# Kernel tuning notes

Hardware: AMD Instinct MI355X
Metric: run time of the kernel (lower is better)

The kernel has to match this reference:

```python
import jax, jax.numpy as jnp
import numpy as np


def _cdist(a, b):
    # Euclidean distance between rows of a [M,D] and b [K,D] -> [M,K]
    a2 = jnp.sum(a * a, axis=-1)[:, None]
    b2 = jnp.sum(b * b, axis=-1)[None, :]
    d2 = a2 + b2 - 2.0 * (a @ b.T)
    return jnp.sqrt(jnp.maximum(d2, 1e-12))


def setup_inputs() -> dict:
    key = jax.random.key(0)
    k1, k2, k3 = jax.random.split(key, 3)
    L, N1, N2, P, D = 2, 8, 8, 1024, 768  # 2 output layers, 32x32 patches, ViT-B dim
    feats = jax.random.normal(k1, (L, N1, P, D), dtype=jnp.float32)
    nfeats = jax.random.normal(k2, (L, N2, P, D), dtype=jnp.float32)
    background_mask = jax.random.uniform(k3, (N1, P), dtype=jnp.float32)
    return {
        "feats": feats,
        "nfeats": nfeats,
        "background_mask": background_mask,
        "img_h": 512,
        "img_w": 512,
        "patch_size": 16,
    }


def reference(feats, nfeats, background_mask, img_h, img_w, patch_size):
    L, N1, P, D = feats.shape
    N2 = nfeats.shape[1]
    PH = img_h // patch_size
    PW = img_w // patch_size

    # L2-normalize patch features (as in Model.forward)
    f = feats / jnp.linalg.norm(feats, axis=-1, keepdims=True)
    nf = nfeats / jnp.linalg.norm(nfeats, axis=-1, keepdims=True)

    scores_list, pixel_list = [], []
    for l in range(L):  # small fixed number of output layers
        a = f[l].reshape(N1 * P, D)
        b = nf[l].reshape(N2 * P, D)
        # [N1,P,N2,P] -> [N1,N2,P,P], halved as in the original
        d = _cdist(a, b).reshape(N1, P, N2, P).transpose(0, 2, 1, 3) / 2.0
        sp = jnp.min(d, axis=-1)                       # [N1,N2,P] nearest normal patch
        sp = sp * background_mask[:, None, :]          # mask background patches
        sc = jnp.mean(jnp.max(sp, axis=-1), axis=-1)   # [N1] image score
        spatch = jnp.mean(sp, axis=1).reshape(N1, PH, PW)
        # bilinear, align_corners=False (half-pixel centers)
        spix = jax.image.resize(spatch, (N1, img_h, img_w), method="bilinear")
        scores_list.append(sc)
        pixel_list.append(spix)

    scores = jnp.mean(jnp.stack(scores_list, axis=0), axis=0)        # [N1]
    scores_pixel = jnp.mean(jnp.stack(pixel_list, axis=0), axis=0)   # [N1,H,W]
    return scores, scores_pixel
```

## Files before the change

kernel.cpp:

```cpp
#include <hip/hip_runtime.h>
#include <hip/hip_bf16.h>

using bf16 = __hip_bfloat16;
typedef __attribute__((ext_vector_type(8))) short short8;
typedef __attribute__((ext_vector_type(4))) float f32x4;

#define NLAY 2
#define NN1 8
#define NN2 8
#define PP 1024
#define DD 768
#define MROWS (NN1*PP)
#define BM 256
#define BN 256
#define BK 64
#define NKT (DD/BK)
#define NCT (MROWS/BN)

__global__ __launch_bounds__(256) void normalize_kernel(
    const float* __restrict__ in, bf16* __restrict__ out, int nrows) {
  int row  = blockIdx.x * 4 + (threadIdx.x >> 6);
  int lane = threadIdx.x & 63;
  if (row >= nrows) return;
  const float* src = in + (size_t)row * DD;
  float4 v[3];
  float ss = 0.f;
#pragma unroll
  for (int i = 0; i < 3; i++) {
    v[i] = *reinterpret_cast<const float4*>(src + lane * 4 + i * 256);
    ss += v[i].x * v[i].x + v[i].y * v[i].y + v[i].z * v[i].z + v[i].w * v[i].w;
  }
#pragma unroll
  for (int off = 1; off < 64; off <<= 1) ss += __shfl_xor(ss, off);
  float rn = rsqrtf(ss);
  bf16* dst = out + (size_t)row * DD;
#pragma unroll
  for (int i = 0; i < 3; i++) {
    bf16 tmp[4];
    tmp[0] = __float2bfloat16(v[i].x * rn);
    tmp[1] = __float2bfloat16(v[i].y * rn);
    tmp[2] = __float2bfloat16(v[i].z * rn);
    tmp[3] = __float2bfloat16(v[i].w * rn);
    *reinterpret_cast<uint2*>(dst + lane * 4 + i * 256) =
        *reinterpret_cast<const uint2*>(tmp);
  }
}


__device__ __forceinline__ short8 ld_frag(const bf16* h, int r, int kc8) {
  return *reinterpret_cast<const short8*>(h + r * 64 + (((kc8) ^ (r & 7)) << 3));
}

#define STAGE(Gbase, Lds) do {                                                  \
  _Pragma("unroll")                                                             \
  for (int i_ = 0; i_ < 2; i_++) {                                              \
    int u_ = i_ * 512 + t;                                                      \
    int r_ = u_ >> 3, s_ = u_ & 7;                                              \
    int sc_ = ((s_ ^ (r_ & 7)) << 3);                                           \
    __builtin_amdgcn_global_load_lds(                                           \
      (const __attribute__((address_space(1))) void*)((Gbase) + (size_t)r_ * DD + sc_), \
      (__attribute__((address_space(3))) void*)((Lds) + u_ * 8), 16, 0, 0);     \
  } } while (0)

#define VM4 asm volatile("s_waitcnt vmcnt(4)" ::: "memory")

#define PHASE(buf, qm, qn, STG, VMC) do {                                       \
  short8 af_[4][2], bf_[2][2];                                                  \
  _Pragma("unroll")                                                             \
  for (int m_ = 0; m_ < 4; m_++)                                                \
    _Pragma("unroll")                                                           \
    for (int ks_ = 0; ks_ < 2; ks_++)                                           \
      af_[m_][ks_] = ld_frag(&As[buf][qm][0], wr * 64 + m_ * 16 + rrow, ks_ * 4 + krow); \
  _Pragma("unroll")                                                             \
  for (int n_ = 0; n_ < 2; n_++)                                                \
    _Pragma("unroll")                                                           \
    for (int ks_ = 0; ks_ < 2; ks_++)                                           \
      bf_[n_][ks_] = ld_frag(&Bs[buf][qn][0], wc * 32 + n_ * 16 + rrow, ks_ * 4 + krow); \
  STG;                                                                          \
  __builtin_amdgcn_s_barrier();                                                 \
  asm volatile("s_waitcnt lgkmcnt(0)" ::: "memory");                            \
  __builtin_amdgcn_s_setprio(1);                                                \
  _Pragma("unroll")                                                             \
  for (int m_ = 0; m_ < 4; m_++)                                                \
    _Pragma("unroll")                                                           \
    for (int n_ = 0; n_ < 2; n_++)                                              \
      _Pragma("unroll")                                                         \
      for (int ks_ = 0; ks_ < 2; ks_++)                                         \
        acc[(qm) * 4 + m_][(qn) * 2 + n_] = __builtin_amdgcn_mfma_f32_16x16x32_bf16( \
            af_[m_][ks_], bf_[n_][ks_], acc[(qm) * 4 + m_][(qn) * 2 + n_], 0, 0, 0); \
  __builtin_amdgcn_s_setprio(0);                                                \
  VMC;                                                                          \
  __builtin_amdgcn_s_barrier();                                                 \
} while (0)

__global__ __launch_bounds__(512, 2) void gemm_max_kernel(
    const bf16* __restrict__ A, const bf16* __restrict__ Bm,
    float* __restrict__ partials) {
  __shared__ bf16 As[2][2][128 * 64];
  __shared__ bf16 Bs[2][2][128 * 64];
  __shared__ float red[4][256];

  const int l     = blockIdx.z;
  const int tilec = blockIdx.x;
  const int tiler = blockIdx.y;
  const bf16* Ab = A  + ((size_t)l * MROWS + (size_t)tiler * BM) * DD;
  const bf16* Bb = Bm + ((size_t)l * MROWS + (size_t)tilec * BN) * DD;

  const int t    = threadIdx.x;
  const int lane = t & 63;
  const int wave = t >> 6;
  const int wr   = wave >> 2;
  const int wc   = wave & 3;
  const int rrow = lane & 15;
  const int krow = lane >> 4;

  f32x4 acc[8][4];
#pragma unroll
  for (int m = 0; m < 8; m++)
#pragma unroll
    for (int n = 0; n < 4; n++) acc[m][n] = (f32x4){0.f, 0.f, 0.f, 0.f};

  STAGE(Ab,                         &As[0][0][0]);
  STAGE(Bb,                         &Bs[0][0][0]);
  STAGE(Ab + (size_t)128 * DD,      &As[0][1][0]);
  STAGE(Bb + (size_t)128 * DD,      &Bs[0][1][0]);
  STAGE(Ab + BK,                    &As[1][0][0]);
  STAGE(Bb + BK,                    &Bs[1][0][0]);
  VM4;
  __builtin_amdgcn_s_barrier();

  for (int i = 0; i < NKT / 2; i++) {
    const int ktP = 2 * i + 1;
    const int ktE = 2 * i + 2;
    const int ktO = 2 * i + 3;
    PHASE(0, 0, 0, STAGE(Ab + (size_t)128 * DD + (size_t)ktP * BK, &As[1][1][0]), (void)0);
    PHASE(0, 0, 1, STAGE(Bb + (size_t)128 * DD + (size_t)ktP * BK, &Bs[1][1][0]), (void)0);
    PHASE(0, 1, 0, if (ktE < NKT) STAGE(Ab + (size_t)ktE * BK, &As[0][0][0]), (void)0);
    PHASE(0, 1, 1, if (ktE < NKT) STAGE(Bb + (size_t)ktE * BK, &Bs[0][0][0]), VM4);
    PHASE(1, 0, 0, if (ktE < NKT) STAGE(Ab + (size_t)128 * DD + (size_t)ktE * BK, &As[0][1][0]), (void)0);
    PHASE(1, 0, 1, if (ktE < NKT) STAGE(Bb + (size_t)128 * DD + (size_t)ktE * BK, &Bs[0][1][0]), (void)0);
    PHASE(1, 1, 0, if (ktO < NKT) STAGE(Ab + (size_t)ktO * BK, &As[1][0][0]), (void)0);
    PHASE(1, 1, 1, if (ktO < NKT) STAGE(Bb + (size_t)ktO * BK, &Bs[1][0][0]), VM4);
  }

#pragma unroll
  for (int m = 0; m < 8; m++) {
#pragma unroll
    for (int j = 0; j < 4; j++) {
      float v = acc[m][0][j];
      v = fmaxf(v, acc[m][1][j]);
      v = fmaxf(v, acc[m][2][j]);
      v = fmaxf(v, acc[m][3][j]);
#pragma unroll
      for (int off = 1; off < 16; off <<= 1) v = fmaxf(v, __shfl_xor(v, off));
      if (rrow == 0) {
        int row = (m >> 2) * 128 + wr * 64 + (m & 3) * 16 + krow * 4 + j;
        red[wc][row] = v;
      }
    }
  }
  __syncthreads();
  if (t < 256) {
    float v = fmaxf(fmaxf(red[0][t], red[1][t]), fmaxf(red[2][t], red[3][t]));
    partials[((size_t)l * MROWS + (size_t)tiler * BM + t) * NCT + tilec] = v;
  }
}

__global__ __launch_bounds__(1024) void reduce_kernel(
    const float* __restrict__ partials, const float* __restrict__ mask,
    float* __restrict__ scores, float* __restrict__ spatch) {
  const int n1 = blockIdx.x;
  const int p  = threadIdx.x;
  const int row = n1 * PP + p;
  const float mk = mask[row];

  float sp[16];
  float ssum = 0.f;
#pragma unroll
  for (int l = 0; l < NLAY; l++) {
    const float* pr = partials + ((size_t)l * MROWS + row) * NCT;
#pragma unroll
    for (int n2 = 0; n2 < NN2; n2++) {
      float md = pr[n2 * 4];
#pragma unroll
      for (int tt = 1; tt < 4; tt++) md = fmaxf(md, pr[n2 * 4 + tt]);
      float d2 = fmaxf(2.f - 2.f * md, 1e-12f);
      float s  = 0.5f * sqrtf(d2) * mk;
      sp[l * 8 + n2] = s;
      ssum += s;
    }
  }
  spatch[row] = ssum * (1.f / 16.f);

  __shared__ float wred[16][16];
  __shared__ float sres[16];
  const int lane = p & 63;
  const int wave = p >> 6;
#pragma unroll
  for (int v = 0; v < 16; v++) {
    float x = sp[v];
#pragma unroll
    for (int off = 1; off < 64; off <<= 1) x = fmaxf(x, __shfl_xor(x, off));
    if (lane == 0) wred[wave][v] = x;
  }
  __syncthreads();
  if (p < 16) {
    float x = wred[0][p];
#pragma unroll
    for (int w = 1; w < 16; w++) x = fmaxf(x, wred[w][p]);
    sres[p] = x;
  }
  __syncthreads();
  if (p == 0) {
    float s = 0.f;
#pragma unroll
    for (int v = 0; v < 16; v++) s += sres[v];
    scores[n1] = s * (1.f / 16.f);
  }
}

__global__ __launch_bounds__(256) void upsample_kernel(
    const float* __restrict__ spatch, float* __restrict__ out) {
  int idx = blockIdx.x * 256 + threadIdx.x;
  if (idx >= NN1 * 512 * 512) return;
  int x = idx & 511;
  int y = (idx >> 9) & 511;
  int n = idx >> 18;
  float sx = (x + 0.5f) * 0.0625f - 0.5f;
  float sy = (y + 0.5f) * 0.0625f - 0.5f;
  int x0 = (int)floorf(sx); float wx = sx - (float)x0;
  int y0 = (int)floorf(sy); float wy = sy - (float)y0;
  int x1 = min(x0 + 1, 31); x0 = max(x0, 0);
  int y1 = min(y0 + 1, 31); y0 = max(y0, 0);
  const float* s = spatch + n * PP;
  float v00 = s[y0 * 32 + x0], v01 = s[y0 * 32 + x1];
  float v10 = s[y1 * 32 + x0], v11 = s[y1 * 32 + x1];
  float v = (1.f - wy) * ((1.f - wx) * v00 + wx * v01) +
            wy * ((1.f - wx) * v10 + wx * v11);
  out[idx] = v;
}

extern "C" void kernel_launch(void* const* d_in, const int* in_sizes, int n_in,
                              void* d_out, int out_size, void* d_ws, size_t ws_size,
                              hipStream_t stream) {
  const float* feats  = (const float*)d_in[0];
  const float* nfeats = (const float*)d_in[1];
  const float* mask   = (const float*)d_in[2];
  float* out = (float*)d_out;

  bf16* Abf = (bf16*)d_ws;
  bf16* Bbf = Abf + (size_t)NLAY * MROWS * DD;
  float* partials = (float*)(Bbf + (size_t)NLAY * MROWS * DD);
  float* spatch   = partials + (size_t)NLAY * MROWS * NCT;

  normalize_kernel<<<(NLAY * MROWS) / 4, 256, 0, stream>>>(feats,  Abf, NLAY * MROWS);
  normalize_kernel<<<(NLAY * MROWS) / 4, 256, 0, stream>>>(nfeats, Bbf, NLAY * MROWS);

  dim3 g(NCT, MROWS / BM, NLAY);
  gemm_max_kernel<<<g, 512, 0, stream>>>(Abf, Bbf, partials);

  reduce_kernel<<<NN1, 1024, 0, stream>>>(partials, mask, out, spatch);

  upsample_kernel<<<(NN1 * 512 * 512) / 256, 256, 0, stream>>>(spatch, out + 8);
}
```

Measured before the change: 392.8 us.

## Switch GEMM to 32x32x16 MFMA, XCD-aware tile mapping, fuse normalize launches

The fused GEMM+row-max kernel now uses 32x32x16 bf16 MFMAs instead of 16x16x32. Each wave now covers a 64-row by 64-column slice of one B half, with a reworked A/B fragment load order and staging schedule. Blocks are launched on a 1D grid remapped so that tiles sharing A rows and the same layer land on the same XCD, aimed at better L2 reuse. The two normalize launches are merged into one. The risks are higher register pressure from the 16-wide accumulators and a more intricate waitcnt schedule.

```diff
diff --git a/kernel.cpp b/kernel.cpp
--- a/kernel.cpp
+++ b/kernel.cpp
@@ -3,7 +3,7 @@
 
 using bf16 = __hip_bfloat16;
 typedef __attribute__((ext_vector_type(8))) short short8;
-typedef __attribute__((ext_vector_type(4))) float f32x4;
+typedef __attribute__((ext_vector_type(16))) float f32x16;
 
 #define NLAY 2
 #define NN1 8
@@ -18,11 +18,15 @@
 #define NCT (MROWS/BN)
 
 __global__ __launch_bounds__(256) void normalize_kernel(
-    const float* __restrict__ in, bf16* __restrict__ out, int nrows) {
+    const float* __restrict__ in0, const float* __restrict__ in1,
+    bf16* __restrict__ out0, bf16* __restrict__ out1) {
   int row  = blockIdx.x * 4 + (threadIdx.x >> 6);
   int lane = threadIdx.x & 63;
-  if (row >= nrows) return;
-  const float* src = in + (size_t)row * DD;
+  const int half = NLAY * MROWS;
+  const float* src;
+  bf16* dst;
+  if (row < half) { src = in0 + (size_t)row * DD;          dst = out0 + (size_t)row * DD; }
+  else            { src = in1 + (size_t)(row - half) * DD; dst = out1 + (size_t)(row - half) * DD; }
   float4 v[3];
   float ss = 0.f;
 #pragma unroll
@@ -33,7 +37,6 @@
 #pragma unroll
   for (int off = 1; off < 64; off <<= 1) ss += __shfl_xor(ss, off);
   float rn = rsqrtf(ss);
-  bf16* dst = out + (size_t)row * DD;
 #pragma unroll
   for (int i = 0; i < 3; i++) {
     bf16 tmp[4];
@@ -47,8 +50,8 @@
 }
 
 
-__device__ __forceinline__ short8 ld_frag(const bf16* h, int r, int kc8) {
-  return *reinterpret_cast<const short8*>(h + r * 64 + (((kc8) ^ (r & 7)) << 3));
+__device__ __forceinline__ short8 ld_frag(const bf16* h, int r, int slot) {
+  return *reinterpret_cast<const short8*>(h + r * 64 + (((slot) ^ (r & 7)) << 3));
 }
 
 #define STAGE(Gbase, Lds) do {                                                  \
@@ -62,33 +65,44 @@
       (__attribute__((address_space(3))) void*)((Lds) + u_ * 8), 16, 0, 0);     \
   } } while (0)
 
-#define VM4 asm volatile("s_waitcnt vmcnt(4)" ::: "memory")
-
-#define PHASE(buf, qm, qn, STG, VMC) do {                                       \
-  short8 af_[4][2], bf_[2][2];                                                  \
-  _Pragma("unroll")                                                             \
-  for (int m_ = 0; m_ < 4; m_++)                                                \
-    _Pragma("unroll")                                                           \
-    for (int ks_ = 0; ks_ < 2; ks_++)                                           \
-      af_[m_][ks_] = ld_frag(&As[buf][qm][0], wr * 64 + m_ * 16 + rrow, ks_ * 4 + krow); \
-  _Pragma("unroll")                                                             \
-  for (int n_ = 0; n_ < 2; n_++)                                                \
-    _Pragma("unroll")                                                           \
-    for (int ks_ = 0; ks_ < 2; ks_++)                                           \
-      bf_[n_][ks_] = ld_frag(&Bs[buf][qn][0], wc * 32 + n_ * 16 + rrow, ks_ * 4 + krow); \
+#define VM2 asm volatile("s_waitcnt vmcnt(2)" ::: "memory")
+#define VM0 asm volatile("s_waitcnt vmcnt(0)" ::: "memory")
+
+#define LOAD_AF(buf, qm, kp)                                                    \
+  _Pragma("unroll") for (int mt_ = 0; mt_ < 2; mt_++)                           \
+  _Pragma("unroll") for (int j_ = 0; j_ < 2; j_++)                              \
+    af_[mt_][j_] = ld_frag(&As[buf][qm][0], wr * 64 + mt_ * 32 + l31, ((kp) * 2 + j_) * 2 + hi);
+
+#define LOAD_BF(buf, kp)                                                        \
+  _Pragma("unroll") for (int n_ = 0; n_ < 2; n_++)                              \
+  _Pragma("unroll") for (int j_ = 0; j_ < 2; j_++)                              \
+    bf_[n_][j_] = ld_frag(&Bs[buf][hB][0], wcin * 64 + n_ * 32 + l31, ((kp) * 2 + j_) * 2 + hi);
+
+#define MFMAS(qm)                                                               \
+  __builtin_amdgcn_s_setprio(1);                                                \
+  _Pragma("unroll") for (int j_ = 0; j_ < 2; j_++)                              \
+  _Pragma("unroll") for (int mt_ = 0; mt_ < 2; mt_++)                           \
+  _Pragma("unroll") for (int n_ = 0; n_ < 2; n_++)                              \
+    acc[(qm) * 2 + mt_][n_] = __builtin_amdgcn_mfma_f32_32x32x16_bf16(          \
+        af_[mt_][j_], bf_[n_][j_], acc[(qm) * 2 + mt_][n_], 0, 0, 0);           \
+  __builtin_amdgcn_s_setprio(0);
+
+#define PHASE_Q0(buf, kp, STG, VMC) do {                                        \
+  LOAD_BF(buf, kp); LOAD_AF(buf, 0, kp);                                        \
   STG;                                                                          \
   __builtin_amdgcn_s_barrier();                                                 \
   asm volatile("s_waitcnt lgkmcnt(0)" ::: "memory");                            \
-  __builtin_amdgcn_s_setprio(1);                                                \
-  _Pragma("unroll")                                                             \
-  for (int m_ = 0; m_ < 4; m_++)                                                \
-    _Pragma("unroll")                                                           \
-    for (int n_ = 0; n_ < 2; n_++)                                              \
-      _Pragma("unroll")                                                         \
-      for (int ks_ = 0; ks_ < 2; ks_++)                                         \
-        acc[(qm) * 4 + m_][(qn) * 2 + n_] = __builtin_amdgcn_mfma_f32_16x16x32_bf16( \
-            af_[m_][ks_], bf_[n_][ks_], acc[(qm) * 4 + m_][(qn) * 2 + n_], 0, 0, 0); \
-  __builtin_amdgcn_s_setprio(0);                                                \
+  MFMAS(0);                                                                     \
+  VMC;                                                                          \
+  __builtin_amdgcn_s_barrier();                                                 \
+} while (0)
+
+#define PHASE_Q1(buf, kp, STG, VMC) do {                                        \
+  LOAD_AF(buf, 1, kp);                                                          \
+  STG;                                                                          \
+  __builtin_amdgcn_s_barrier();                                                 \
+  asm volatile("s_waitcnt lgkmcnt(0)" ::: "memory");                            \
+  MFMAS(1);                                                                     \
   VMC;                                                                          \
   __builtin_amdgcn_s_barrier();                                                 \
 } while (0)
@@ -100,9 +114,13 @@
   __shared__ bf16 Bs[2][2][128 * 64];
   __shared__ float red[4][256];
 
-  const int l     = blockIdx.z;
-  const int tilec = blockIdx.x;
-  const int tiler = blockIdx.y;
+  const int id  = blockIdx.x;
+  const int xcd = id & 7, p = id >> 3;
+  const int l     = xcd >> 2;
+  const int q     = p & 31, rnd = p >> 5;
+  const int tiler = (xcd & 3) * 8 + (q & 7);
+  const int tilec = rnd * 4 + (q >> 3);
+
   const bf16* Ab = A  + ((size_t)l * MROWS + (size_t)tiler * BM) * DD;
   const bf16* Bb = Bm + ((size_t)l * MROWS + (size_t)tilec * BN) * DD;
 
@@ -111,50 +129,50 @@
   const int wave = t >> 6;
   const int wr   = wave >> 2;
   const int wc   = wave & 3;
-  const int rrow = lane & 15;
-  const int krow = lane >> 4;
-
-  f32x4 acc[8][4];
-#pragma unroll
-  for (int m = 0; m < 8; m++)
-#pragma unroll
-    for (int n = 0; n < 4; n++) acc[m][n] = (f32x4){0.f, 0.f, 0.f, 0.f};
-
-  STAGE(Ab,                         &As[0][0][0]);
-  STAGE(Bb,                         &Bs[0][0][0]);
-  STAGE(Ab + (size_t)128 * DD,      &As[0][1][0]);
-  STAGE(Bb + (size_t)128 * DD,      &Bs[0][1][0]);
-  STAGE(Ab + BK,                    &As[1][0][0]);
-  STAGE(Bb + BK,                    &Bs[1][0][0]);
-  VM4;
+  const int hB   = wc >> 1;
+  const int wcin = wc & 1;
+  const int l31  = lane & 31;
+  const int hi   = lane >> 5;
+
+  f32x16 acc[4][2];
+#pragma unroll
+  for (int a = 0; a < 4; a++)
+#pragma unroll
+    for (int n = 0; n < 2; n++)
+#pragma unroll
+      for (int j = 0; j < 16; j++) acc[a][n][j] = 0.f;
+
+  STAGE(Ab,                      &As[0][0][0]);
+  STAGE(Ab + (size_t)128 * DD,   &As[0][1][0]);
+  STAGE(Bb,                      &Bs[0][0][0]);
+  STAGE(Bb + (size_t)128 * DD,   &Bs[0][1][0]);
+  STAGE(Ab + BK,                 &As[1][0][0]);
+  VM2;
   __builtin_amdgcn_s_barrier();
 
   for (int i = 0; i < NKT / 2; i++) {
-    const int ktP = 2 * i + 1;
-    const int ktE = 2 * i + 2;
-    const int ktO = 2 * i + 3;
-    PHASE(0, 0, 0, STAGE(Ab + (size_t)128 * DD + (size_t)ktP * BK, &As[1][1][0]), (void)0);
-    PHASE(0, 0, 1, STAGE(Bb + (size_t)128 * DD + (size_t)ktP * BK, &Bs[1][1][0]), (void)0);
-    PHASE(0, 1, 0, if (ktE < NKT) STAGE(Ab + (size_t)ktE * BK, &As[0][0][0]), (void)0);
-    PHASE(0, 1, 1, if (ktE < NKT) STAGE(Bb + (size_t)ktE * BK, &Bs[0][0][0]), VM4);
-    PHASE(1, 0, 0, if (ktE < NKT) STAGE(Ab + (size_t)128 * DD + (size_t)ktE * BK, &As[0][1][0]), (void)0);
-    PHASE(1, 0, 1, if (ktE < NKT) STAGE(Bb + (size_t)128 * DD + (size_t)ktE * BK, &Bs[0][1][0]), (void)0);
-    PHASE(1, 1, 0, if (ktO < NKT) STAGE(Ab + (size_t)ktO * BK, &As[1][0][0]), (void)0);
-    PHASE(1, 1, 1, if (ktO < NKT) STAGE(Bb + (size_t)ktO * BK, &Bs[1][0][0]), VM4);
-  }
-
-#pragma unroll
-  for (int m = 0; m < 8; m++) {
-#pragma unroll
-    for (int j = 0; j < 4; j++) {
-      float v = acc[m][0][j];
-      v = fmaxf(v, acc[m][1][j]);
-      v = fmaxf(v, acc[m][2][j]);
-      v = fmaxf(v, acc[m][3][j]);
-#pragma unroll
-      for (int off = 1; off < 16; off <<= 1) v = fmaxf(v, __shfl_xor(v, off));
-      if (rrow == 0) {
-        int row = (m >> 2) * 128 + wr * 64 + (m & 3) * 16 + krow * 4 + j;
+    const int O = 2 * i + 1, NE = 2 * i + 2, NO = 2 * i + 3;
+    short8 af_[2][2], bf_[2][2];
+    PHASE_Q0(0, 0, STAGE(Bb + (size_t)O * BK,                    &Bs[1][0][0]), (void)0);
+    PHASE_Q1(0, 0, STAGE(Bb + (size_t)128 * DD + (size_t)O * BK, &Bs[1][1][0]), (void)0);
+    PHASE_Q0(0, 1, STAGE(Ab + (size_t)128 * DD + (size_t)O * BK, &As[1][1][0]), (void)0);
+    PHASE_Q1(0, 1, if (NE < NKT) STAGE(Ab + (size_t)NE * BK, &As[0][0][0]),
+             if (NE < NKT) { VM2; } else { VM0; });
+    PHASE_Q0(1, 0, if (NE < NKT) STAGE(Bb + (size_t)NE * BK, &Bs[0][0][0]), (void)0);
+    PHASE_Q1(1, 0, if (NE < NKT) STAGE(Bb + (size_t)128 * DD + (size_t)NE * BK, &Bs[0][1][0]), (void)0);
+    PHASE_Q0(1, 1, if (NE < NKT) STAGE(Ab + (size_t)128 * DD + (size_t)NE * BK, &As[0][1][0]), (void)0);
+    PHASE_Q1(1, 1, if (NO < NKT) STAGE(Ab + (size_t)NO * BK, &As[1][0][0]), VM2);
+  }
+
+#pragma unroll
+  for (int a = 0; a < 4; a++) {
+#pragma unroll
+    for (int j = 0; j < 16; j++) {
+      float v = fmaxf(acc[a][0][j], acc[a][1][j]);
+#pragma unroll
+      for (int off = 1; off < 32; off <<= 1) v = fmaxf(v, __shfl_xor(v, off));
+      if (l31 == 0) {
+        int row = (a >> 1) * 128 + wr * 64 + (a & 1) * 32 + (j & 3) + 8 * (j >> 2) + 4 * hi;
         red[wc][row] = v;
       }
     }
@@ -253,11 +271,9 @@
   float* partials = (float*)(Bbf + (size_t)NLAY * MROWS * DD);
   float* spatch   = partials + (size_t)NLAY * MROWS * NCT;
 
-  normalize_kernel<<<(NLAY * MROWS) / 4, 256, 0, stream>>>(feats,  Abf, NLAY * MROWS);
-  normalize_kernel<<<(NLAY * MROWS) / 4, 256, 0, stream>>>(nfeats, Bbf, NLAY * MROWS);
-
-  dim3 g(NCT, MROWS / BM, NLAY);
-  gemm_max_kernel<<<g, 512, 0, stream>>>(Abf, Bbf, partials);
+  normalize_kernel<<<(2 * NLAY * MROWS) / 4, 256, 0, stream>>>(feats, nfeats, Abf, Bbf);
+
+  gemm_max_kernel<<<NCT * (MROWS / BM) * NLAY, 512, 0, stream>>>(Abf, Bbf, partials);
 
   reduce_kernel<<<NN1, 1024, 0, stream>>>(partials, mask, out, spatch);
 
```

Measured after the change: 438.4 us. +11.6%, slower.
